# Kernel tuning notes

Measured on AMD Instinct MI355X. Metric: run time of the kernel, lower is better.

## Reference

```python
import jax, jax.numpy as jnp
import numpy as np

ZDIM, NF, H, S, B = 64, 32, 256, 256, 1024


def setup_inputs() -> dict:
    key = jax.random.key(0)
    ks = jax.random.split(key, 8)
    def w(k, shape, fan):
        return (jax.random.normal(k, shape, jnp.float32) / np.sqrt(fan)).astype(jnp.float32)
    return {
        "z": jax.random.normal(ks[0], (B, ZDIM), jnp.float32),
        "W_lat": w(ks[1], (2 * H, ZDIM), ZDIM),
        "b_lat": jnp.zeros((2 * H,), jnp.float32),
        "W_ih": w(ks[2], (4 * H, NF), NF),
        "b_ih": jnp.zeros((4 * H,), jnp.float32),
        "W_hh": w(ks[3], (4 * H, H), H),
        "b_hh": jnp.zeros((4 * H,), jnp.float32),
        "W_out": w(ks[4], (NF, H), H),
        "b_out": jnp.zeros((NF,), jnp.float32),
        "W_sig": w(ks[5], (NF, H * S), H * S),
        "b_sig": jnp.zeros((NF,), jnp.float32),
    }


def reference(z, W_lat, b_lat, W_ih, b_ih, W_hh, b_hh, W_out, b_out, W_sig, b_sig):
    # from_latent: split into initial hidden / cell state
    hc = z @ W_lat.T + b_lat                      # [B, 2H]
    h, c = hc[:, :H], hc[:, H:]
    x = jnp.zeros((z.shape[0], NF), z.dtype)      # initial LSTM input
    bias = b_ih + b_hh                            # fold both LSTM biases

    def step(carry, _):
        h, c, x = carry
        g = x @ W_ih.T + h @ W_hh.T + bias        # [B, 4H]; torch gate order i,f,g,o
        i, f, gg, o = jnp.split(g, 4, axis=-1)
        c = jax.nn.sigmoid(f) * c + jax.nn.sigmoid(i) * jnp.tanh(gg)
        h = jax.nn.sigmoid(o) * jnp.tanh(c)
        x_next = jnp.tanh(h) @ W_out.T + b_out    # activation(Tanh) then from_lstm
        return (h, c, x_next), (h, x_next)

    _, (hs, mus) = jax.lax.scan(step, (h, c, x), None, length=S)
    # mus: [S, B, NF] -> mu: [B, NF, S]
    mu = jnp.transpose(mus, (1, 2, 0))
    # hs: [S, B, H] -> [B, H, S] -> flatten hidden-major, matching torch permute+reshape
    xs = jnp.transpose(hs, (1, 2, 0)).reshape(-1, H * S)
    sigma = jax.nn.softplus(xs @ W_sig.T + b_sig)[:, :, None]   # [B, NF, 1]
    return (mu, sigma)
```

## Files before the change

kernel.cpp:

```cpp
#include <hip/hip_runtime.h>

#define NF 32
#define HDIM 256
#define SLEN 256
#define BATCH 1024

typedef float f32x4 __attribute__((ext_vector_type(4)));
typedef __bf16 bf16x8 __attribute__((ext_vector_type(8)));
typedef unsigned short u16;

#define MFMA __builtin_amdgcn_mfma_f32_16x16x32_bf16

#define WHH_O 0
#define WIH_O 32768
#define WOUT_O 36864
#define WLAT_O 37888
#define PREP1_N 41984
#define WT_BYTE (1u << 20)
#define HST_BYTE (8u << 20)

__device__ __forceinline__ u16 f2bf(float x) {
  __bf16 b = (__bf16)x;
  return __builtin_bit_cast(u16, b);
}
__device__ __forceinline__ unsigned int pk2(float a, float b) {
  return (unsigned int)f2bf(a) | ((unsigned int)f2bf(b) << 16);
}
__device__ __forceinline__ float sigf(float x) {
  return __fdividef(1.0f, 1.0f + __expf(-x));
}
__device__ __forceinline__ float tanhf_(float x) {
  return 1.0f - __fdividef(2.0f, __expf(2.0f * x) + 1.0f);
}

__device__ __forceinline__ void wg_barrier_lds() {
  asm volatile("s_waitcnt lgkmcnt(0)" ::: "memory");
  __builtin_amdgcn_s_barrier();
}

__global__ void prep_weights(const float* __restrict__ Whh, const float* __restrict__ Wih,
                             const float* __restrict__ Wout, const float* __restrict__ Wlat,
                             uint4* __restrict__ ws) {
  int i = blockIdx.x * 256 + threadIdx.x;
  if (i >= PREP1_N) return;
  int l = i & 63;
  int c16 = l & 15, g4 = l >> 4;
  const float* src;
  if (i < WIH_O) {
    int t = (i >> 6) & 7, j = i >> 9;
    src = Whh + (j * 16 + c16) * 256 + t * 32 + 8 * g4;
  } else if (i < WOUT_O) {
    int ii = i - WIH_O;
    int j = ii >> 6;
    src = Wih + (j * 16 + c16) * 32 + 8 * g4;
  } else if (i < WLAT_O) {
    int ii = i - WOUT_O;
    int t = (ii >> 6) & 7, j = ii >> 9;
    src = Wout + (j * 16 + c16) * 256 + t * 32 + 8 * g4;
  } else {
    int ii = i - WLAT_O;
    int t = (ii >> 6) & 1, j = ii >> 7;
    src = Wlat + (j * 16 + c16) * 64 + t * 32 + 8 * g4;
  }
  uint4 P;
  P.x = pk2(src[0], src[1]);
  P.y = pk2(src[2], src[3]);
  P.z = pk2(src[4], src[5]);
  P.w = pk2(src[6], src[7]);
  ws[i] = P;
}

__global__ void prep_wt(const float* __restrict__ Wsig, unsigned short* __restrict__ Wt) {
  __shared__ float tile[32][257];
  int f = blockIdx.x >> 3, hb = blockIdx.x & 7;
  int tid = threadIdx.x;
  const float* src = Wsig + f * (HDIM * SLEN) + hb * 32 * 256;
#pragma unroll
  for (int i = 0; i < 32; ++i) tile[i][tid] = src[i * 256 + tid];
  __syncthreads();
  int s = tid;
  unsigned short tmp[32];
#pragma unroll
  for (int h = 0; h < 32; ++h) tmp[h] = f2bf(tile[h][s]);
  uint4* dst = (uint4*)(Wt + f * 65536 + s * 256 + hb * 32);
  const uint4* tsrc = (const uint4*)tmp;
#pragma unroll
  for (int j = 0; j < 4; ++j) dst[j] = tsrc[j];
}

__global__ __launch_bounds__(1024, 4) void lstm_scan(
    const float* __restrict__ z, const float* __restrict__ b_lat,
    const float* __restrict__ b_ih, const float* __restrict__ b_hh,
    const float* __restrict__ b_out,
    const uint4* __restrict__ ws, unsigned short* __restrict__ hst,
    float* __restrict__ out) {
  __shared__ __align__(16) uint4 wihl[4096];
  __shared__ __align__(16) uint4 woutb[1024];
  __shared__ __align__(16) u16 hbuf[2][16][256];
  __shared__ __align__(16) u16 thbuf[16][256];
  __shared__ __align__(16) u16 xbuf[2][16][32];
  __shared__ __align__(16) float mubuf[16][16][32];

  const int tid = threadIdx.x, w = tid >> 6, l = tid & 63;
  const int c16 = l & 15, g4 = l >> 4, r0 = g4 * 4;
  const int wg = blockIdx.x;
  const int swz = (c16 & 7) << 3;

  for (int i = tid; i < 4096; i += 1024) wihl[i] = ws[WIH_O + i];
  if (tid < 1024) woutb[tid] = ws[WOUT_O + tid];

  const uint4* bs[4];
#pragma unroll
  for (int gi = 0; gi < 4; ++gi)
    bs[gi] = ws + WHH_O + ((gi * 16 + w) * 8 + 4) * 64 + l;

  float biasv[4];
#pragma unroll
  for (int gi = 0; gi < 4; ++gi) {
    int n = (gi * 16 + w) * 16 + c16;
    biasv[gi] = b_ih[n] + b_hh[n];
  }
  const int jn = w - 14;
  const float bo = (w >= 14) ? b_out[jn * 16 + c16] : 0.f;

  thbuf[tid >> 6][tid & 63] = f2bf(z[(wg * 16 + (tid >> 6)) * 64 + (tid & 63)]);
  if (tid < 512) xbuf[0][tid >> 5][tid & 31] = 0;
  __syncthreads();

  float cst[4];
  {
    bf16x8 za0 = *reinterpret_cast<const bf16x8*>(&thbuf[c16][8 * g4]);
    bf16x8 za1 = *reinterpret_cast<const bf16x8*>(&thbuf[c16][32 + 8 * g4]);
    float blh = b_lat[w * 16 + c16];
    float blc = b_lat[256 + w * 16 + c16];
    f32x4 ah = {blh, blh, blh, blh}, ac = {blc, blc, blc, blc};
    ah = MFMA(za0, *reinterpret_cast<const bf16x8*>(ws + WLAT_O + (w * 2 + 0) * 64 + l), ah, 0, 0, 0);
    ah = MFMA(za1, *reinterpret_cast<const bf16x8*>(ws + WLAT_O + (w * 2 + 1) * 64 + l), ah, 0, 0, 0);
    ac = MFMA(za0, *reinterpret_cast<const bf16x8*>(ws + WLAT_O + ((16 + w) * 2 + 0) * 64 + l), ac, 0, 0, 0);
    ac = MFMA(za1, *reinterpret_cast<const bf16x8*>(ws + WLAT_O + ((16 + w) * 2 + 1) * 64 + l), ac, 0, 0, 0);
    const int hc = w * 16 + c16;
#pragma unroll
    for (int v = 0; v < 4; ++v) {
      cst[v] = ac[v];
      int rr = r0 + v;
      hbuf[0][rr][hc ^ ((rr & 7) << 3)] = f2bf(ah[v]);
    }
  }
  __syncthreads();

  uint4 pf0[4], pf1[4];
#pragma unroll
  for (int gi = 0; gi < 4; ++gi) pf0[gi] = bs[gi][(0 - 4) * 64];
#pragma unroll
  for (int gi = 0; gi < 4; ++gi) pf1[gi] = bs[gi][(1 - 4) * 64];

  for (int s = 0; s < SLEN; ++s) {
    const int pb = s & 1;
    f32x4 acc[4];
#pragma unroll
    for (int gi = 0; gi < 4; ++gi)
      acc[gi] = (f32x4){biasv[gi], biasv[gi], biasv[gi], biasv[gi]};
#pragma unroll
    for (int kt = 0; kt < 8; ++kt) {
      uint4 pf2[4];
      const int ktn = (kt + 2) & 7;
#pragma unroll
      for (int gi = 0; gi < 4; ++gi) pf2[gi] = bs[gi][(ktn - 4) * 64];
      bf16x8 afr = *reinterpret_cast<const bf16x8*>(&hbuf[pb][c16][(kt * 32 + 8 * g4) ^ swz]);
#pragma unroll
      for (int gi = 0; gi < 4; ++gi)
        acc[gi] = MFMA(afr, __builtin_bit_cast(bf16x8, pf0[gi]), acc[gi], 0, 0, 0);
#pragma unroll
      for (int gi = 0; gi < 4; ++gi) { pf0[gi] = pf1[gi]; pf1[gi] = pf2[gi]; }
    }
    {
      bf16x8 xfr = *reinterpret_cast<const bf16x8*>(&xbuf[pb][c16][8 * g4]);
#pragma unroll
      for (int gi = 0; gi < 4; ++gi)
        acc[gi] = MFMA(xfr, *reinterpret_cast<const bf16x8*>(&wihl[(gi * 16 + w) * 64 + l]), acc[gi], 0, 0, 0);
    }
    {
      const int hc = w * 16 + c16;
#pragma unroll
      for (int v = 0; v < 4; ++v) {
        float iv = acc[0][v];
        float fv = acc[1][v];
        float gv = acc[2][v];
        float ov = acc[3][v];
        float cc = sigf(fv) * cst[v] + sigf(iv) * tanhf_(gv);
        cst[v] = cc;
        float hh = sigf(ov) * tanhf_(cc);
        float th = tanhf_(hh);
        int rr = r0 + v;
        int sc = hc ^ ((rr & 7) << 3);
        hbuf[pb ^ 1][rr][sc] = f2bf(hh);
        thbuf[rr][sc] = f2bf(th);
      }
    }
    wg_barrier_lds();
    if (w >= 14) {
      f32x4 xacc = {bo, bo, bo, bo};
#pragma unroll
      for (int t = 0; t < 8; ++t) {
        bf16x8 ta = *reinterpret_cast<const bf16x8*>(&thbuf[c16][(t * 32 + 8 * g4) ^ swz]);
        xacc = MFMA(ta, *reinterpret_cast<const bf16x8*>(&woutb[(jn * 8 + t) * 64 + l]), xacc, 0, 0, 0);
      }
      const int f = jn * 16 + c16;
      const int sw = s & 15;
#pragma unroll
      for (int v = 0; v < 4; ++v) {
        int rr = r0 + v;
        xbuf[pb ^ 1][rr][f] = f2bf(xacc[v]);
        mubuf[sw][rr][f] = xacc[v];
      }
    } else if (w < 8) {
      int r = tid >> 5;
      int h0 = (tid & 31) * 8;
      uint4 d = *reinterpret_cast<const uint4*>(&hbuf[pb ^ 1][r][h0 ^ ((r & 7) << 3)]);
      *reinterpret_cast<uint4*>(hst + ((wg * 16 + r) << 16) + (s << 8) + h0) = d;
    }
    wg_barrier_lds();
    if ((s & 15) == 15 && tid < 512) {
      int b = tid >> 5, f = tid & 31;
      float* dst = out + ((wg * 16 + b) << 13) + (f << 8) + (s - 15);
#pragma unroll
      for (int j4 = 0; j4 < 4; ++j4) {
        f32x4 vv;
#pragma unroll
        for (int jj = 0; jj < 4; ++jj) vv[jj] = mubuf[j4 * 4 + jj][b][f];
        *reinterpret_cast<f32x4*>(dst + j4 * 4) = vv;
      }
    }
  }
}

__global__ __launch_bounds__(512) void sigma_gemm(
    const unsigned short* __restrict__ hst, const unsigned short* __restrict__ Wt,
    const float* __restrict__ b_sig, float* __restrict__ out) {
  __shared__ float sred[8][16][32];
  const int tid = threadIdx.x;
  const int w = tid >> 6;
  const int l = tid & 63;
  const int c16 = l & 15;
  const int g4 = l >> 4;
  const int wg = blockIdx.x;

  const unsigned short* ap =
      hst + (((wg << 2) + (c16 & 3)) << 16) + ((w * 32) << 8) + (g4 << 3);
  const unsigned short* bp0 = Wt + (c16 << 16) + ((w * 32) << 8) + (g4 << 3);
  const unsigned short* bp1 = Wt + ((16 + c16) << 16) + ((w * 32) << 8) + (g4 << 3);

  f32x4 a0 = {0.f, 0.f, 0.f, 0.f}, a1 = {0.f, 0.f, 0.f, 0.f};
#pragma unroll 8
  for (int kk = 0; kk < 256; ++kk) {
    int off = ((kk >> 3) << 8) + ((kk & 7) << 5);
    bf16x8 av = *reinterpret_cast<const bf16x8*>(ap + off);
    a0 = MFMA(av, *reinterpret_cast<const bf16x8*>(bp0 + off), a0, 0, 0, 0);
    a1 = MFMA(av, *reinterpret_cast<const bf16x8*>(bp1 + off), a1, 0, 0, 0);
  }
#pragma unroll
  for (int v = 0; v < 4; ++v) {
    sred[w][g4 * 4 + v][c16] = a0[v];
    sred[w][g4 * 4 + v][16 + c16] = a1[v];
  }
  __syncthreads();
  int b = tid >> 5, f = tid & 31;
  if (b < 4) {
    float acc = b_sig[f];
#pragma unroll
    for (int ww = 0; ww < 8; ++ww) acc += sred[ww][b][f];
    float sp = fmaxf(acc, 0.0f) + log1pf(__expf(-fabsf(acc)));
    out[BATCH * NF * SLEN + ((wg << 2) + b) * NF + f] = sp;
  }
}

extern "C" void kernel_launch(void* const* d_in, const int* in_sizes, int n_in,
                              void* d_out, int out_size, void* d_ws, size_t ws_size,
                              hipStream_t stream) {
  (void)in_sizes; (void)n_in; (void)out_size; (void)ws_size;
  const float* z     = (const float*)d_in[0];
  const float* W_lat = (const float*)d_in[1];
  const float* b_lat = (const float*)d_in[2];
  const float* W_ih  = (const float*)d_in[3];
  const float* b_ih  = (const float*)d_in[4];
  const float* W_hh  = (const float*)d_in[5];
  const float* b_hh  = (const float*)d_in[6];
  const float* W_out = (const float*)d_in[7];
  const float* b_out = (const float*)d_in[8];
  const float* W_sig = (const float*)d_in[9];
  const float* b_sig = (const float*)d_in[10];
  char* wsb = (char*)d_ws;
  uint4* ws = (uint4*)wsb;
  unsigned short* Wt  = (unsigned short*)(wsb + WT_BYTE);
  unsigned short* hst = (unsigned short*)(wsb + HST_BYTE);
  float* out = (float*)d_out;

  prep_weights<<<(PREP1_N + 255) / 256, 256, 0, stream>>>(W_hh, W_ih, W_out, W_lat, ws);
  prep_wt<<<256, 256, 0, stream>>>(W_sig, Wt);
  lstm_scan<<<64, 1024, 0, stream>>>(z, b_lat, b_ih, b_hh, b_out, ws, hst, out);
  sigma_gemm<<<256, 512, 0, stream>>>(hst, Wt, b_sig, out);
}
```

Before: 2.934 ms.

## Skew output projection and h store to overlap with next step's recurrent GEMM

Result: slower. 4.417 ms (+50.6%).

```diff
diff --git a/kernel.cpp b/kernel.cpp
--- a/kernel.cpp
+++ b/kernel.cpp
@@ -10,6 +10,7 @@
 typedef unsigned short u16;
 
 #define MFMA __builtin_amdgcn_mfma_f32_16x16x32_bf16
+#define BC(x) __builtin_bit_cast(bf16x8, x)
 
 #define WHH_O 0
 #define WIH_O 32768
@@ -32,7 +33,6 @@
 __device__ __forceinline__ float tanhf_(float x) {
   return 1.0f - __fdividef(2.0f, __expf(2.0f * x) + 1.0f);
 }
-
 __device__ __forceinline__ void wg_barrier_lds() {
   asm volatile("s_waitcnt lgkmcnt(0)" ::: "memory");
   __builtin_amdgcn_s_barrier();
@@ -98,7 +98,7 @@
   __shared__ __align__(16) uint4 woutb[1024];
   __shared__ __align__(16) u16 hbuf[2][16][256];
   __shared__ __align__(16) u16 thbuf[16][256];
-  __shared__ __align__(16) u16 xbuf[2][16][32];
+  __shared__ __align__(16) u16 xbuf[16][32];
   __shared__ __align__(16) float mubuf[16][16][32];
 
   const int tid = threadIdx.x, w = tid >> 6, l = tid & 63;
@@ -109,10 +109,10 @@
   for (int i = tid; i < 4096; i += 1024) wihl[i] = ws[WIH_O + i];
   if (tid < 1024) woutb[tid] = ws[WOUT_O + tid];
 
-  const uint4* bs[4];
-#pragma unroll
-  for (int gi = 0; gi < 4; ++gi)
-    bs[gi] = ws + WHH_O + ((gi * 16 + w) * 8 + 4) * 64 + l;
+  const uint4* bs0 = ws + WHH_O + ((0 * 16 + w) * 8 + 4) * 64 + l;
+  const uint4* bs1 = ws + WHH_O + ((1 * 16 + w) * 8 + 4) * 64 + l;
+  const uint4* bs2 = ws + WHH_O + ((2 * 16 + w) * 8 + 4) * 64 + l;
+  const uint4* bs3 = ws + WHH_O + ((3 * 16 + w) * 8 + 4) * 64 + l;
 
   float biasv[4];
 #pragma unroll
@@ -122,9 +122,17 @@
   }
   const int jn = w - 14;
   const float bo = (w >= 14) ? b_out[jn * 16 + c16] : 0.f;
+  const int hc = w * 16 + c16;
+
+  const int eo0 = (0 * 32 + 8 * g4) ^ swz, eo1 = (1 * 32 + 8 * g4) ^ swz;
+  const int eo2 = (2 * 32 + 8 * g4) ^ swz, eo3 = (3 * 32 + 8 * g4) ^ swz;
+  const int eo4 = (4 * 32 + 8 * g4) ^ swz, eo5 = (5 * 32 + 8 * g4) ^ swz;
+  const int eo6 = (6 * 32 + 8 * g4) ^ swz, eo7 = (7 * 32 + 8 * g4) ^ swz;
+  const int so0 = hc ^ (((r0 + 0) & 7) << 3), so1 = hc ^ (((r0 + 1) & 7) << 3);
+  const int so2 = hc ^ (((r0 + 2) & 7) << 3), so3 = hc ^ (((r0 + 3) & 7) << 3);
 
   thbuf[tid >> 6][tid & 63] = f2bf(z[(wg * 16 + (tid >> 6)) * 64 + (tid & 63)]);
-  if (tid < 512) xbuf[0][tid >> 5][tid & 31] = 0;
+  if (tid < 512) xbuf[tid >> 5][tid & 31] = 0;
   __syncthreads();
 
   float cst[4];
@@ -138,99 +146,146 @@
     ah = MFMA(za1, *reinterpret_cast<const bf16x8*>(ws + WLAT_O + (w * 2 + 1) * 64 + l), ah, 0, 0, 0);
     ac = MFMA(za0, *reinterpret_cast<const bf16x8*>(ws + WLAT_O + ((16 + w) * 2 + 0) * 64 + l), ac, 0, 0, 0);
     ac = MFMA(za1, *reinterpret_cast<const bf16x8*>(ws + WLAT_O + ((16 + w) * 2 + 1) * 64 + l), ac, 0, 0, 0);
-    const int hc = w * 16 + c16;
-#pragma unroll
-    for (int v = 0; v < 4; ++v) {
-      cst[v] = ac[v];
-      int rr = r0 + v;
-      hbuf[0][rr][hc ^ ((rr & 7) << 3)] = f2bf(ah[v]);
+    cst[0] = ac[0]; cst[1] = ac[1]; cst[2] = ac[2]; cst[3] = ac[3];
+    hbuf[0][r0 + 0][so0] = f2bf(ah[0]);
+    hbuf[0][r0 + 1][so1] = f2bf(ah[1]);
+    hbuf[0][r0 + 2][so2] = f2bf(ah[2]);
+    hbuf[0][r0 + 3][so3] = f2bf(ah[3]);
+  }
+  __syncthreads();
+
+  uint4 pf0[4], pf1[4], pf2[4], pf3[4];
+#define LOADPF(PF, OFF) \
+  PF[0] = bs0[(OFF) * 64]; PF[1] = bs1[(OFF) * 64]; \
+  PF[2] = bs2[(OFF) * 64]; PF[3] = bs3[(OFF) * 64];
+  LOADPF(pf0, -4) LOADPF(pf1, -3) LOADPF(pf2, -2) LOADPF(pf3, -1)
+
+#define GKT(PB, EO, PF, LOFF) { \
+    bf16x8 afr = *reinterpret_cast<const bf16x8*>(&hbuf[PB][c16][EO]); \
+    acc[0] = MFMA(afr, BC(PF[0]), acc[0], 0, 0, 0); \
+    acc[1] = MFMA(afr, BC(PF[1]), acc[1], 0, 0, 0); \
+    acc[2] = MFMA(afr, BC(PF[2]), acc[2], 0, 0, 0); \
+    acc[3] = MFMA(afr, BC(PF[3]), acc[3], 0, 0, 0); \
+    LOADPF(PF, LOFF) }
+
+#define STEP(PB, S_) { \
+    const int s_ = (S_); \
+    f32x4 acc[4]; \
+    acc[0] = (f32x4){biasv[0], biasv[0], biasv[0], biasv[0]}; \
+    acc[1] = (f32x4){biasv[1], biasv[1], biasv[1], biasv[1]}; \
+    acc[2] = (f32x4){biasv[2], biasv[2], biasv[2], biasv[2]}; \
+    acc[3] = (f32x4){biasv[3], biasv[3], biasv[3], biasv[3]}; \
+    f32x4 xacc = {bo, bo, bo, bo}; \
+     \
+    if (w >= 14 && s_ > 0) { \
+      xacc = MFMA(*reinterpret_cast<const bf16x8*>(&thbuf[c16][eo0]), BC(woutb[(jn * 8 + 0) * 64 + l]), xacc, 0, 0, 0); \
+      xacc = MFMA(*reinterpret_cast<const bf16x8*>(&thbuf[c16][eo1]), BC(woutb[(jn * 8 + 1) * 64 + l]), xacc, 0, 0, 0); \
+      xacc = MFMA(*reinterpret_cast<const bf16x8*>(&thbuf[c16][eo2]), BC(woutb[(jn * 8 + 2) * 64 + l]), xacc, 0, 0, 0); \
+      xacc = MFMA(*reinterpret_cast<const bf16x8*>(&thbuf[c16][eo3]), BC(woutb[(jn * 8 + 3) * 64 + l]), xacc, 0, 0, 0); \
+      xacc = MFMA(*reinterpret_cast<const bf16x8*>(&thbuf[c16][eo4]), BC(woutb[(jn * 8 + 4) * 64 + l]), xacc, 0, 0, 0); \
+      xacc = MFMA(*reinterpret_cast<const bf16x8*>(&thbuf[c16][eo5]), BC(woutb[(jn * 8 + 5) * 64 + l]), xacc, 0, 0, 0); \
+      xacc = MFMA(*reinterpret_cast<const bf16x8*>(&thbuf[c16][eo6]), BC(woutb[(jn * 8 + 6) * 64 + l]), xacc, 0, 0, 0); \
+      xacc = MFMA(*reinterpret_cast<const bf16x8*>(&thbuf[c16][eo7]), BC(woutb[(jn * 8 + 7) * 64 + l]), xacc, 0, 0, 0); \
+      const int f = jn * 16 + c16; \
+      xbuf[r0 + 0][f] = f2bf(xacc[0]); \
+      xbuf[r0 + 1][f] = f2bf(xacc[1]); \
+      xbuf[r0 + 2][f] = f2bf(xacc[2]); \
+      xbuf[r0 + 3][f] = f2bf(xacc[3]); \
+    } \
+    __builtin_amdgcn_s_setprio(1); \
+    GKT(PB, eo0, pf0, 0) GKT(PB, eo1, pf1, 1) GKT(PB, eo2, pf2, 2) GKT(PB, eo3, pf3, 3) \
+    GKT(PB, eo4, pf0, -4) GKT(PB, eo5, pf1, -3) GKT(PB, eo6, pf2, -2) GKT(PB, eo7, pf3, -1) \
+    __builtin_amdgcn_s_setprio(0); \
+    if (w >= 6 && w < 14 && s_ > 0) { \
+      int task = (w - 6) * 64 + l; \
+      int r = task >> 5, h0 = (task & 31) * 8; \
+      uint4 d = *reinterpret_cast<const uint4*>(&hbuf[PB][r][h0 ^ ((r & 7) << 3)]); \
+      *reinterpret_cast<uint4*>(hst + ((wg * 16 + r) << 16) + ((s_ - 1) << 8) + h0) = d; \
+    } \
+    wg_barrier_lds();  \
+    { \
+      bf16x8 xfr = *reinterpret_cast<const bf16x8*>(&xbuf[c16][8 * g4]); \
+      acc[0] = MFMA(xfr, BC(wihl[(0 * 16 + w) * 64 + l]), acc[0], 0, 0, 0); \
+      acc[1] = MFMA(xfr, BC(wihl[(1 * 16 + w) * 64 + l]), acc[1], 0, 0, 0); \
+      acc[2] = MFMA(xfr, BC(wihl[(2 * 16 + w) * 64 + l]), acc[2], 0, 0, 0); \
+      acc[3] = MFMA(xfr, BC(wihl[(3 * 16 + w) * 64 + l]), acc[3], 0, 0, 0); \
+    } \
+    { \
+      float iv, fv, gv, ov, cc, hh, th; \
+      iv = acc[0][0]; fv = acc[1][0]; gv = acc[2][0]; ov = acc[3][0]; \
+      cc = sigf(fv) * cst[0] + sigf(iv) * tanhf_(gv); cst[0] = cc; \
+      hh = sigf(ov) * tanhf_(cc); th = tanhf_(hh); \
+      hbuf[PB ^ 1][r0 + 0][so0] = f2bf(hh); thbuf[r0 + 0][so0] = f2bf(th); \
+      iv = acc[0][1]; fv = acc[1][1]; gv = acc[2][1]; ov = acc[3][1]; \
+      cc = sigf(fv) * cst[1] + sigf(iv) * tanhf_(gv); cst[1] = cc; \
+      hh = sigf(ov) * tanhf_(cc); th = tanhf_(hh); \
+      hbuf[PB ^ 1][r0 + 1][so1] = f2bf(hh); thbuf[r0 + 1][so1] = f2bf(th); \
+      iv = acc[0][2]; fv = acc[1][2]; gv = acc[2][2]; ov = acc[3][2]; \
+      cc = sigf(fv) * cst[2] + sigf(iv) * tanhf_(gv); cst[2] = cc; \
+      hh = sigf(ov) * tanhf_(cc); th = tanhf_(hh); \
+      hbuf[PB ^ 1][r0 + 2][so2] = f2bf(hh); thbuf[r0 + 2][so2] = f2bf(th); \
+      iv = acc[0][3]; fv = acc[1][3]; gv = acc[2][3]; ov = acc[3][3]; \
+      cc = sigf(fv) * cst[3] + sigf(iv) * tanhf_(gv); cst[3] = cc; \
+      hh = sigf(ov) * tanhf_(cc); th = tanhf_(hh); \
+      hbuf[PB ^ 1][r0 + 3][so3] = f2bf(hh); thbuf[r0 + 3][so3] = f2bf(th); \
+    } \
+    if (w >= 14 && s_ > 0) { \
+      const int f = jn * 16 + c16, mi = (s_ - 1) & 15; \
+      mubuf[mi][r0 + 0][f] = xacc[0]; \
+      mubuf[mi][r0 + 1][f] = xacc[1]; \
+      mubuf[mi][r0 + 2][f] = xacc[2]; \
+      mubuf[mi][r0 + 3][f] = xacc[3]; \
+    } \
+    wg_barrier_lds();  \
+    if ((s_ & 15) == 0 && s_ > 0 && tid < 512) { \
+      int b = tid >> 5, f = tid & 31; \
+      float* dst = out + ((wg * 16 + b) << 13) + (f << 8) + (s_ - 16); \
+      _Pragma("unroll") for (int j4 = 0; j4 < 4; ++j4) { \
+        f32x4 vv; \
+        _Pragma("unroll") for (int jj = 0; jj < 4; ++jj) vv[jj] = mubuf[j4 * 4 + jj][b][f]; \
+        *reinterpret_cast<f32x4*>(dst + j4 * 4) = vv; \
+      } \
+    } \
+  }
+
+  for (int sp = 0; sp < 128; ++sp) {
+    STEP(0, 2 * sp)
+    STEP(1, 2 * sp + 1)
+  }
+
+  if (w >= 14) {
+    f32x4 xacc = {bo, bo, bo, bo};
+    xacc = MFMA(*reinterpret_cast<const bf16x8*>(&thbuf[c16][eo0]), BC(woutb[(jn * 8 + 0) * 64 + l]), xacc, 0, 0, 0);
+    xacc = MFMA(*reinterpret_cast<const bf16x8*>(&thbuf[c16][eo1]), BC(woutb[(jn * 8 + 1) * 64 + l]), xacc, 0, 0, 0);
+    xacc = MFMA(*reinterpret_cast<const bf16x8*>(&thbuf[c16][eo2]), BC(woutb[(jn * 8 + 2) * 64 + l]), xacc, 0, 0, 0);
+    xacc = MFMA(*reinterpret_cast<const bf16x8*>(&thbuf[c16][eo3]), BC(woutb[(jn * 8 + 3) * 64 + l]), xacc, 0, 0, 0);
+    xacc = MFMA(*reinterpret_cast<const bf16x8*>(&thbuf[c16][eo4]), BC(woutb[(jn * 8 + 4) * 64 + l]), xacc, 0, 0, 0);
+    xacc = MFMA(*reinterpret_cast<const bf16x8*>(&thbuf[c16][eo5]), BC(woutb[(jn * 8 + 5) * 64 + l]), xacc, 0, 0, 0);
+    xacc = MFMA(*reinterpret_cast<const bf16x8*>(&thbuf[c16][eo6]), BC(woutb[(jn * 8 + 6) * 64 + l]), xacc, 0, 0, 0);
+    xacc = MFMA(*reinterpret_cast<const bf16x8*>(&thbuf[c16][eo7]), BC(woutb[(jn * 8 + 7) * 64 + l]), xacc, 0, 0, 0);
+    const int f = jn * 16 + c16;
+    mubuf[15][r0 + 0][f] = xacc[0];
+    mubuf[15][r0 + 1][f] = xacc[1];
+    mubuf[15][r0 + 2][f] = xacc[2];
+    mubuf[15][r0 + 3][f] = xacc[3];
+  }
+  __syncthreads();
+  if (tid < 512) {
+    int b = tid >> 5, f = tid & 31;
+    float* dst = out + ((wg * 16 + b) << 13) + (f << 8) + 240;
+#pragma unroll
+    for (int j4 = 0; j4 < 4; ++j4) {
+      f32x4 vv;
+#pragma unroll
+      for (int jj = 0; jj < 4; ++jj) vv[jj] = mubuf[j4 * 4 + jj][b][f];
+      *reinterpret_cast<f32x4*>(dst + j4 * 4) = vv;
     }
   }
-  __syncthreads();
-
-  uint4 pf0[4], pf1[4];
-#pragma unroll
-  for (int gi = 0; gi < 4; ++gi) pf0[gi] = bs[gi][(0 - 4) * 64];
-#pragma unroll
-  for (int gi = 0; gi < 4; ++gi) pf1[gi] = bs[gi][(1 - 4) * 64];
-
-  for (int s = 0; s < SLEN; ++s) {
-    const int pb = s & 1;
-    f32x4 acc[4];
-#pragma unroll
-    for (int gi = 0; gi < 4; ++gi)
-      acc[gi] = (f32x4){biasv[gi], biasv[gi], biasv[gi], biasv[gi]};
-#pragma unroll
-    for (int kt = 0; kt < 8; ++kt) {
-      uint4 pf2[4];
-      const int ktn = (kt + 2) & 7;
-#pragma unroll
-      for (int gi = 0; gi < 4; ++gi) pf2[gi] = bs[gi][(ktn - 4) * 64];
-      bf16x8 afr = *reinterpret_cast<const bf16x8*>(&hbuf[pb][c16][(kt * 32 + 8 * g4) ^ swz]);
-#pragma unroll
-      for (int gi = 0; gi < 4; ++gi)
-        acc[gi] = MFMA(afr, __builtin_bit_cast(bf16x8, pf0[gi]), acc[gi], 0, 0, 0);
-#pragma unroll
-      for (int gi = 0; gi < 4; ++gi) { pf0[gi] = pf1[gi]; pf1[gi] = pf2[gi]; }
-    }
-    {
-      bf16x8 xfr = *reinterpret_cast<const bf16x8*>(&xbuf[pb][c16][8 * g4]);
-#pragma unroll
-      for (int gi = 0; gi < 4; ++gi)
-        acc[gi] = MFMA(xfr, *reinterpret_cast<const bf16x8*>(&wihl[(gi * 16 + w) * 64 + l]), acc[gi], 0, 0, 0);
-    }
-    {
-      const int hc = w * 16 + c16;
-#pragma unroll
-      for (int v = 0; v < 4; ++v) {
-        float iv = acc[0][v];
-        float fv = acc[1][v];
-        float gv = acc[2][v];
-        float ov = acc[3][v];
-        float cc = sigf(fv) * cst[v] + sigf(iv) * tanhf_(gv);
-        cst[v] = cc;
-        float hh = sigf(ov) * tanhf_(cc);
-        float th = tanhf_(hh);
-        int rr = r0 + v;
-        int sc = hc ^ ((rr & 7) << 3);
-        hbuf[pb ^ 1][rr][sc] = f2bf(hh);
-        thbuf[rr][sc] = f2bf(th);
-      }
-    }
-    wg_barrier_lds();
-    if (w >= 14) {
-      f32x4 xacc = {bo, bo, bo, bo};
-#pragma unroll
-      for (int t = 0; t < 8; ++t) {
-        bf16x8 ta = *reinterpret_cast<const bf16x8*>(&thbuf[c16][(t * 32 + 8 * g4) ^ swz]);
-        xacc = MFMA(ta, *reinterpret_cast<const bf16x8*>(&woutb[(jn * 8 + t) * 64 + l]), xacc, 0, 0, 0);
-      }
-      const int f = jn * 16 + c16;
-      const int sw = s & 15;
-#pragma unroll
-      for (int v = 0; v < 4; ++v) {
-        int rr = r0 + v;
-        xbuf[pb ^ 1][rr][f] = f2bf(xacc[v]);
-        mubuf[sw][rr][f] = xacc[v];
-      }
-    } else if (w < 8) {
-      int r = tid >> 5;
-      int h0 = (tid & 31) * 8;
-      uint4 d = *reinterpret_cast<const uint4*>(&hbuf[pb ^ 1][r][h0 ^ ((r & 7) << 3)]);
-      *reinterpret_cast<uint4*>(hst + ((wg * 16 + r) << 16) + (s << 8) + h0) = d;
-    }
-    wg_barrier_lds();
-    if ((s & 15) == 15 && tid < 512) {
-      int b = tid >> 5, f = tid & 31;
-      float* dst = out + ((wg * 16 + b) << 13) + (f << 8) + (s - 15);
-#pragma unroll
-      for (int j4 = 0; j4 < 4; ++j4) {
-        f32x4 vv;
-#pragma unroll
-        for (int jj = 0; jj < 4; ++jj) vv[jj] = mubuf[j4 * 4 + jj][b][f];
-        *reinterpret_cast<f32x4*>(dst + j4 * 4) = vv;
-      }
-    }
+  if (w < 8) {
+    int r = tid >> 5;
+    int h0 = (tid & 31) * 8;
+    uint4 d = *reinterpret_cast<const uint4*>(&hbuf[0][r][h0 ^ ((r & 7) << 3)]);
+    *reinterpret_cast<uint4*>(hst + ((wg * 16 + r) << 16) + (255 << 8) + h0) = d;
   }
 }
 
```

## Keep recurrent LSTM weights resident in registers with 512-thread blocks

Applied to the files above, without the earlier changes.

Result: slower. 3.444 ms (+17.4%).

```diff
diff --git a/kernel.cpp b/kernel.cpp
--- a/kernel.cpp
+++ b/kernel.cpp
@@ -10,6 +10,7 @@
 typedef unsigned short u16;
 
 #define MFMA __builtin_amdgcn_mfma_f32_16x16x32_bf16
+#define BC(x) __builtin_bit_cast(bf16x8, x)
 
 #define WHH_O 0
 #define WIH_O 32768
@@ -32,7 +33,6 @@
 __device__ __forceinline__ float tanhf_(float x) {
   return 1.0f - __fdividef(2.0f, __expf(2.0f * x) + 1.0f);
 }
-
 __device__ __forceinline__ void wg_barrier_lds() {
   asm volatile("s_waitcnt lgkmcnt(0)" ::: "memory");
   __builtin_amdgcn_s_barrier();
@@ -88,13 +88,12 @@
   for (int j = 0; j < 4; ++j) dst[j] = tsrc[j];
 }
 
-__global__ __launch_bounds__(1024, 4) void lstm_scan(
+__global__ __launch_bounds__(512, 1) void lstm_scan(
     const float* __restrict__ z, const float* __restrict__ b_lat,
     const float* __restrict__ b_ih, const float* __restrict__ b_hh,
     const float* __restrict__ b_out,
     const uint4* __restrict__ ws, unsigned short* __restrict__ hst,
     float* __restrict__ out) {
-  __shared__ __align__(16) uint4 wihl[4096];
   __shared__ __align__(16) uint4 woutb[1024];
   __shared__ __align__(16) u16 hbuf[2][16][256];
   __shared__ __align__(16) u16 thbuf[16][256];
@@ -105,122 +104,165 @@
   const int c16 = l & 15, g4 = l >> 4, r0 = g4 * 4;
   const int wg = blockIdx.x;
   const int swz = (c16 & 7) << 3;
-
-  for (int i = tid; i < 4096; i += 1024) wihl[i] = ws[WIH_O + i];
-  if (tid < 1024) woutb[tid] = ws[WOUT_O + tid];
-
-  const uint4* bs[4];
-#pragma unroll
-  for (int gi = 0; gi < 4; ++gi)
-    bs[gi] = ws + WHH_O + ((gi * 16 + w) * 8 + 4) * 64 + l;
-
-  float biasv[4];
-#pragma unroll
-  for (int gi = 0; gi < 4; ++gi) {
-    int n = (gi * 16 + w) * 16 + c16;
-    biasv[gi] = b_ih[n] + b_hh[n];
-  }
-  const int jn = w - 14;
-  const float bo = (w >= 14) ? b_out[jn * 16 + c16] : 0.f;
-
-  thbuf[tid >> 6][tid & 63] = f2bf(z[(wg * 16 + (tid >> 6)) * 64 + (tid & 63)]);
-  if (tid < 512) xbuf[0][tid >> 5][tid & 31] = 0;
+  const int jjA = 2 * w, jjB = 2 * w + 1;
+
+  if (tid < 1024) { woutb[tid] = ws[WOUT_O + tid]; woutb[tid + 512] = ws[WOUT_O + tid + 512]; }
+
+  uint4 whA[4][8], whB[4][8], wiA[4], wiB[4];
+#pragma unroll
+  for (int g = 0; g < 4; ++g) {
+#pragma unroll
+    for (int kt = 0; kt < 8; ++kt) {
+      whA[g][kt] = ws[WHH_O + ((g * 16 + jjA) * 8 + kt) * 64 + l];
+      whB[g][kt] = ws[WHH_O + ((g * 16 + jjB) * 8 + kt) * 64 + l];
+    }
+    wiA[g] = ws[WIH_O + (g * 16 + jjA) * 64 + l];
+    wiB[g] = ws[WIH_O + (g * 16 + jjB) * 64 + l];
+  }
+
+  float biasA[4], biasB[4];
+#pragma unroll
+  for (int g = 0; g < 4; ++g) {
+    int nA = (g * 16 + jjA) * 16 + c16;
+    int nB = (g * 16 + jjB) * 16 + c16;
+    biasA[g] = b_ih[nA] + b_hh[nA];
+    biasB[g] = b_ih[nB] + b_hh[nB];
+  }
+  const float bo = (w < 2) ? b_out[w * 16 + c16] : 0.f;
+
+  const int eo0 = (0 * 32 + 8 * g4) ^ swz, eo1 = (1 * 32 + 8 * g4) ^ swz;
+  const int eo2 = (2 * 32 + 8 * g4) ^ swz, eo3 = (3 * 32 + 8 * g4) ^ swz;
+  const int eo4 = (4 * 32 + 8 * g4) ^ swz, eo5 = (5 * 32 + 8 * g4) ^ swz;
+  const int eo6 = (6 * 32 + 8 * g4) ^ swz, eo7 = (7 * 32 + 8 * g4) ^ swz;
+  const int ca = jjA * 16 + c16, cb = jjB * 16 + c16;
+  int soA[4], soB[4];
+#pragma unroll
+  for (int v = 0; v < 4; ++v) {
+    soA[v] = ca ^ (((r0 + v) & 7) << 3);
+    soB[v] = cb ^ (((r0 + v) & 7) << 3);
+  }
+
+  for (int idx = tid; idx < 1024; idx += 512)
+    thbuf[idx >> 6][idx & 63] = f2bf(z[(wg * 16 + (idx >> 6)) * 64 + (idx & 63)]);
+  xbuf[0][tid >> 5][tid & 31] = 0;
   __syncthreads();
 
-  float cst[4];
+  float cstA[4], cstB[4];
   {
     bf16x8 za0 = *reinterpret_cast<const bf16x8*>(&thbuf[c16][8 * g4]);
     bf16x8 za1 = *reinterpret_cast<const bf16x8*>(&thbuf[c16][32 + 8 * g4]);
-    float blh = b_lat[w * 16 + c16];
-    float blc = b_lat[256 + w * 16 + c16];
-    f32x4 ah = {blh, blh, blh, blh}, ac = {blc, blc, blc, blc};
-    ah = MFMA(za0, *reinterpret_cast<const bf16x8*>(ws + WLAT_O + (w * 2 + 0) * 64 + l), ah, 0, 0, 0);
-    ah = MFMA(za1, *reinterpret_cast<const bf16x8*>(ws + WLAT_O + (w * 2 + 1) * 64 + l), ah, 0, 0, 0);
-    ac = MFMA(za0, *reinterpret_cast<const bf16x8*>(ws + WLAT_O + ((16 + w) * 2 + 0) * 64 + l), ac, 0, 0, 0);
-    ac = MFMA(za1, *reinterpret_cast<const bf16x8*>(ws + WLAT_O + ((16 + w) * 2 + 1) * 64 + l), ac, 0, 0, 0);
-    const int hc = w * 16 + c16;
+    float bhA = b_lat[ca], bhB = b_lat[cb];
+    float bcA = b_lat[256 + ca], bcB = b_lat[256 + cb];
+    f32x4 ahA = {bhA, bhA, bhA, bhA}, ahB = {bhB, bhB, bhB, bhB};
+    f32x4 acA = {bcA, bcA, bcA, bcA}, acB = {bcB, bcB, bcB, bcB};
+    ahA = MFMA(za0, *reinterpret_cast<const bf16x8*>(ws + WLAT_O + (jjA * 2 + 0) * 64 + l), ahA, 0, 0, 0);
+    ahA = MFMA(za1, *reinterpret_cast<const bf16x8*>(ws + WLAT_O + (jjA * 2 + 1) * 64 + l), ahA, 0, 0, 0);
+    ahB = MFMA(za0, *reinterpret_cast<const bf16x8*>(ws + WLAT_O + (jjB * 2 + 0) * 64 + l), ahB, 0, 0, 0);
+    ahB = MFMA(za1, *reinterpret_cast<const bf16x8*>(ws + WLAT_O + (jjB * 2 + 1) * 64 + l), ahB, 0, 0, 0);
+    acA = MFMA(za0, *reinterpret_cast<const bf16x8*>(ws + WLAT_O + ((16 + jjA) * 2 + 0) * 64 + l), acA, 0, 0, 0);
+    acA = MFMA(za1, *reinterpret_cast<const bf16x8*>(ws + WLAT_O + ((16 + jjA) * 2 + 1) * 64 + l), acA, 0, 0, 0);
+    acB = MFMA(za0, *reinterpret_cast<const bf16x8*>(ws + WLAT_O + ((16 + jjB) * 2 + 0) * 64 + l), acB, 0, 0, 0);
+    acB = MFMA(za1, *reinterpret_cast<const bf16x8*>(ws + WLAT_O + ((16 + jjB) * 2 + 1) * 64 + l), acB, 0, 0, 0);
 #pragma unroll
     for (int v = 0; v < 4; ++v) {
-      cst[v] = ac[v];
-      int rr = r0 + v;
-      hbuf[0][rr][hc ^ ((rr & 7) << 3)] = f2bf(ah[v]);
+      cstA[v] = acA[v]; cstB[v] = acB[v];
+      hbuf[0][r0 + v][soA[v]] = f2bf(ahA[v]);
+      hbuf[0][r0 + v][soB[v]] = f2bf(ahB[v]);
     }
   }
   __syncthreads();
-
-  uint4 pf0[4], pf1[4];
-#pragma unroll
-  for (int gi = 0; gi < 4; ++gi) pf0[gi] = bs[gi][(0 - 4) * 64];
-#pragma unroll
-  for (int gi = 0; gi < 4; ++gi) pf1[gi] = bs[gi][(1 - 4) * 64];
 
   for (int s = 0; s < SLEN; ++s) {
     const int pb = s & 1;
-    f32x4 acc[4];
-#pragma unroll
-    for (int gi = 0; gi < 4; ++gi)
-      acc[gi] = (f32x4){biasv[gi], biasv[gi], biasv[gi], biasv[gi]};
-#pragma unroll
-    for (int kt = 0; kt < 8; ++kt) {
-      uint4 pf2[4];
-      const int ktn = (kt + 2) & 7;
-#pragma unroll
-      for (int gi = 0; gi < 4; ++gi) pf2[gi] = bs[gi][(ktn - 4) * 64];
-      bf16x8 afr = *reinterpret_cast<const bf16x8*>(&hbuf[pb][c16][(kt * 32 + 8 * g4) ^ swz]);
-#pragma unroll
-      for (int gi = 0; gi < 4; ++gi)
-        acc[gi] = MFMA(afr, __builtin_bit_cast(bf16x8, pf0[gi]), acc[gi], 0, 0, 0);
-#pragma unroll
-      for (int gi = 0; gi < 4; ++gi) { pf0[gi] = pf1[gi]; pf1[gi] = pf2[gi]; }
-    }
+    const u16* hrd = &hbuf[pb][0][0];
+
+    f32x4 aA[4], aB[4];
+#pragma unroll
+    for (int g = 0; g < 4; ++g) {
+      aA[g] = (f32x4){biasA[g], biasA[g], biasA[g], biasA[g]};
+      aB[g] = (f32x4){biasB[g], biasB[g], biasB[g], biasB[g]};
+    }
+    __builtin_amdgcn_s_setprio(1);
     {
+      bf16x8 afr;
+      afr = *reinterpret_cast<const bf16x8*>(hrd + c16 * 256 + eo0);
+#pragma unroll
+      for (int g = 0; g < 4; ++g) { aA[g] = MFMA(afr, BC(whA[g][0]), aA[g], 0, 0, 0); aB[g] = MFMA(afr, BC(whB[g][0]), aB[g], 0, 0, 0); }
+      afr = *reinterpret_cast<const bf16x8*>(hrd + c16 * 256 + eo1);
+#pragma unroll
+      for (int g = 0; g < 4; ++g) { aA[g] = MFMA(afr, BC(whA[g][1]), aA[g], 0, 0, 0); aB[g] = MFMA(afr, BC(whB[g][1]), aB[g], 0, 0, 0); }
+      afr = *reinterpret_cast<const bf16x8*>(hrd + c16 * 256 + eo2);
+#pragma unroll
+      for (int g = 0; g < 4; ++g) { aA[g] = MFMA(afr, BC(whA[g][2]), aA[g], 0, 0, 0); aB[g] = MFMA(afr, BC(whB[g][2]), aB[g], 0, 0, 0); }
+      afr = *reinterpret_cast<const bf16x8*>(hrd + c16 * 256 + eo3);
+#pragma unroll
+      for (int g = 0; g < 4; ++g) { aA[g] = MFMA(afr, BC(whA[g][3]), aA[g], 0, 0, 0); aB[g] = MFMA(afr, BC(whB[g][3]), aB[g], 0, 0, 0); }
+      afr = *reinterpret_cast<const bf16x8*>(hrd + c16 * 256 + eo4);
+#pragma unroll
+      for (int g = 0; g < 4; ++g) { aA[g] = MFMA(afr, BC(whA[g][4]), aA[g], 0, 0, 0); aB[g] = MFMA(afr, BC(whB[g][4]), aB[g], 0, 0, 0); }
+      afr = *reinterpret_cast<const bf16x8*>(hrd + c16 * 256 + eo5);
+#pragma unroll
+      for (int g = 0; g < 4; ++g) { aA[g] = MFMA(afr, BC(whA[g][5]), aA[g], 0, 0, 0); aB[g] = MFMA(afr, BC(whB[g][5]), aB[g], 0, 0, 0); }
+      afr = *reinterpret_cast<const bf16x8*>(hrd + c16 * 256 + eo6);
+#pragma unroll
+      for (int g = 0; g < 4; ++g) { aA[g] = MFMA(afr, BC(whA[g][6]), aA[g], 0, 0, 0); aB[g] = MFMA(afr, BC(whB[g][6]), aB[g], 0, 0, 0); }
+      afr = *reinterpret_cast<const bf16x8*>(hrd + c16 * 256 + eo7);
+#pragma unroll
+      for (int g = 0; g < 4; ++g) { aA[g] = MFMA(afr, BC(whA[g][7]), aA[g], 0, 0, 0); aB[g] = MFMA(afr, BC(whB[g][7]), aB[g], 0, 0, 0); }
       bf16x8 xfr = *reinterpret_cast<const bf16x8*>(&xbuf[pb][c16][8 * g4]);
 #pragma unroll
-      for (int gi = 0; gi < 4; ++gi)
-        acc[gi] = MFMA(xfr, *reinterpret_cast<const bf16x8*>(&wihl[(gi * 16 + w) * 64 + l]), acc[gi], 0, 0, 0);
-    }
-    {
-      const int hc = w * 16 + c16;
+      for (int g = 0; g < 4; ++g) { aA[g] = MFMA(xfr, BC(wiA[g]), aA[g], 0, 0, 0); aB[g] = MFMA(xfr, BC(wiB[g]), aB[g], 0, 0, 0); }
+    }
+    __builtin_amdgcn_s_setprio(0);
+
+#pragma unroll
+    for (int v = 0; v < 4; ++v) {
+      float cc, hh, th;
+      cc = sigf(aA[1][v]) * cstA[v] + sigf(aA[0][v]) * tanhf_(aA[2][v]);
+      cstA[v] = cc;
+      hh = sigf(aA[3][v]) * tanhf_(cc);
+      th = tanhf_(hh);
+      hbuf[pb ^ 1][r0 + v][soA[v]] = f2bf(hh);
+      thbuf[r0 + v][soA[v]] = f2bf(th);
+      cc = sigf(aB[1][v]) * cstB[v] + sigf(aB[0][v]) * tanhf_(aB[2][v]);
+      cstB[v] = cc;
+      hh = sigf(aB[3][v]) * tanhf_(cc);
+      th = tanhf_(hh);
+      hbuf[pb ^ 1][r0 + v][soB[v]] = f2bf(hh);
+      thbuf[r0 + v][soB[v]] = f2bf(th);
+    }
+    wg_barrier_lds();
+
+    if (w < 2) {
+      f32x4 xacc = {bo, bo, bo, bo};
+      xacc = MFMA(*reinterpret_cast<const bf16x8*>(&thbuf[c16][eo0]), BC(woutb[(w * 8 + 0) * 64 + l]), xacc, 0, 0, 0);
+      xacc = MFMA(*reinterpret_cast<const bf16x8*>(&thbuf[c16][eo1]), BC(woutb[(w * 8 + 1) * 64 + l]), xacc, 0, 0, 0);
+      xacc = MFMA(*reinterpret_cast<const bf16x8*>(&thbuf[c16][eo2]), BC(woutb[(w * 8 + 2) * 64 + l]), xacc, 0, 0, 0);
+      xacc = MFMA(*reinterpret_cast<const bf16x8*>(&thbuf[c16][eo3]), BC(woutb[(w * 8 + 3) * 64 + l]), xacc, 0, 0, 0);
+      xacc = MFMA(*reinterpret_cast<const bf16x8*>(&thbuf[c16][eo4]), BC(woutb[(w * 8 + 4) * 64 + l]), xacc, 0, 0, 0);
+      xacc = MFMA(*reinterpret_cast<const bf16x8*>(&thbuf[c16][eo5]), BC(woutb[(w * 8 + 5) * 64 + l]), xacc, 0, 0, 0);
+      xacc = MFMA(*reinterpret_cast<const bf16x8*>(&thbuf[c16][eo6]), BC(woutb[(w * 8 + 6) * 64 + l]), xacc, 0, 0, 0);
+      xacc = MFMA(*reinterpret_cast<const bf16x8*>(&thbuf[c16][eo7]), BC(woutb[(w * 8 + 7) * 64 + l]), xacc, 0, 0, 0);
+      const int f = w * 16 + c16;
+      const int sw = s & 15;
 #pragma unroll
       for (int v = 0; v < 4; ++v) {
-        float iv = acc[0][v];
-        float fv = acc[1][v];
-        float gv = acc[2][v];
-        float ov = acc[3][v];
-        float cc = sigf(fv) * cst[v] + sigf(iv) * tanhf_(gv);
-        cst[v] = cc;
-        float hh = sigf(ov) * tanhf_(cc);
-        float th = tanhf_(hh);
-        int rr = r0 + v;
-        int sc = hc ^ ((rr & 7) << 3);
-        hbuf[pb ^ 1][rr][sc] = f2bf(hh);
-        thbuf[rr][sc] = f2bf(th);
+        xbuf[pb ^ 1][r0 + v][f] = f2bf(xacc[v]);
+        mubuf[sw][r0 + v][f] = xacc[v];
       }
+    } else if (w < 6) {
+      int base = (w - 2) * 64 + l;
+#pragma unroll
+      for (int rep = 0; rep < 2; ++rep) {
+        int task = base + rep * 256;
+        int r = task >> 5, h0 = (task & 31) * 8;
+        uint4 d = *reinterpret_cast<const uint4*>(&hbuf[pb ^ 1][r][h0 ^ ((r & 7) << 3)]);
+        *reinterpret_cast<uint4*>(hst + ((wg * 16 + r) << 16) + (s << 8) + h0) = d;
+      }
     }
     wg_barrier_lds();
-    if (w >= 14) {
-      f32x4 xacc = {bo, bo, bo, bo};
-#pragma unroll
-      for (int t = 0; t < 8; ++t) {
-        bf16x8 ta = *reinterpret_cast<const bf16x8*>(&thbuf[c16][(t * 32 + 8 * g4) ^ swz]);
-        xacc = MFMA(ta, *reinterpret_cast<const bf16x8*>(&woutb[(jn * 8 + t) * 64 + l]), xacc, 0, 0, 0);
-      }
-      const int f = jn * 16 + c16;
-      const int sw = s & 15;
-#pragma unroll
-      for (int v = 0; v < 4; ++v) {
-        int rr = r0 + v;
-        xbuf[pb ^ 1][rr][f] = f2bf(xacc[v]);
-        mubuf[sw][rr][f] = xacc[v];
-      }
-    } else if (w < 8) {
-      int r = tid >> 5;
-      int h0 = (tid & 31) * 8;
-      uint4 d = *reinterpret_cast<const uint4*>(&hbuf[pb ^ 1][r][h0 ^ ((r & 7) << 3)]);
-      *reinterpret_cast<uint4*>(hst + ((wg * 16 + r) << 16) + (s << 8) + h0) = d;
-    }
-    wg_barrier_lds();
-    if ((s & 15) == 15 && tid < 512) {
+
+    if ((s & 15) == 15) {
       int b = tid >> 5, f = tid & 31;
       float* dst = out + ((wg * 16 + b) << 13) + (f << 8) + (s - 15);
 #pragma unroll
@@ -297,6 +339,6 @@
 
   prep_weights<<<(PREP1_N + 255) / 256, 256, 0, stream>>>(W_hh, W_ih, W_out, W_lat, ws);
   prep_wt<<<256, 256, 0, stream>>>(W_sig, Wt);
-  lstm_scan<<<64, 1024, 0, stream>>>(z, b_lat, b_ih, b_hh, b_out, ws, hst, out);
+  lstm_scan<<<64, 512, 0, stream>>>(z, b_lat, b_ih, b_hh, b_out, ws, hst, out);
   sigma_gemm<<<256, 512, 0, stream>>>(hst, Wt, b_sig, out);
 }
```
